# Kernel optimization log

Measured on AMD Instinct MI355X. Metric: run time of the kernel, lower is better.

## Reference

```python
import jax, jax.numpy as jnp
import numpy as np

N_NODES = 50000
D_IN = 128
HIDDEN = 128
UNITS_DENSE = 256
N_EDGES = 600000
N_PRED = 200000
N_SEL = 300000


def setup_inputs() -> dict:
    key = jax.random.key(0)
    ks = jax.random.split(key, 12)
    node_state = jax.random.normal(ks[0], (N_NODES, D_IN), jnp.float32)
    edge_index = jax.random.randint(ks[1], (2, N_EDGES), 0, N_NODES, jnp.int32)
    out_edges = jax.random.randint(ks[2], (2, N_PRED), 0, N_NODES, jnp.int32)
    set_idx = jnp.sort(jax.random.randint(ks[3], (N_SEL,), 0, 2 * N_PRED, jnp.int32))
    # Glorot-ish scaled weights
    W1 = jax.random.normal(ks[4], (D_IN, HIDDEN), jnp.float32) / np.float32(np.sqrt(D_IN))
    b1 = jnp.zeros((HIDDEN,), jnp.float32)
    W2 = jax.random.normal(ks[5], (HIDDEN, HIDDEN), jnp.float32) / np.float32(np.sqrt(HIDDEN))
    b2 = jnp.zeros((HIDDEN,), jnp.float32)
    dense_W = jax.random.normal(ks[6], (2 * 0 + HIDDEN, UNITS_DENSE), jnp.float32) / np.float32(np.sqrt(HIDDEN))
    dense_b = jnp.zeros((UNITS_DENSE,), jnp.float32)
    out_W = jax.random.normal(ks[7], (UNITS_DENSE, 2), jnp.float32) / np.float32(np.sqrt(UNITS_DENSE))
    out_b = jnp.zeros((2,), jnp.float32)
    return {
        "node_state": node_state, "edge_index": edge_index, "out_edges": out_edges,
        "set_idx": set_idx, "W1": W1, "b1": b1, "W2": W2, "b2": b2,
        "dense_W": dense_W, "dense_b": dense_b, "out_W": out_W, "out_b": out_b,
    }


def _graph_conv(h, src, dst, W, b):
    """DGL GraphConv, norm='both', no activation: D_in^{-1/2} A D_out^{-1/2} H W + b."""
    n = h.shape[0]
    ones = jnp.ones(src.shape[0], h.dtype)
    deg_out = jnp.clip(jax.ops.segment_sum(ones, src, num_segments=n), 1.0)  # [N]
    deg_in = jnp.clip(jax.ops.segment_sum(ones, dst, num_segments=n), 1.0)   # [N]
    h = (h * jax.lax.rsqrt(deg_out)[:, None]) @ W                            # [N, H]
    agg = jax.ops.segment_sum(h[src], dst, num_segments=n)                   # [N, H]
    return agg * jax.lax.rsqrt(deg_in)[:, None] + b


def reference(node_state, edge_index, out_edges, set_idx,
              W1, b1, W2, b2, dense_W, dense_b, out_W, out_b):
    src, dst = edge_index[0], edge_index[1]
    h = _graph_conv(node_state, src, dst, W1, b1)
    h = _graph_conv(h, src, dst, W2, b2)
    # concat along axis=0 as in the original: [2*E_pred, H]
    edge_state = jnp.concatenate([h[out_edges[0]], h[out_edges[1]]], axis=0)
    # boolean_mask replaced by equivalent gather of selected (True) rows
    edge_state_set = edge_state[set_idx]                                      # [N_SEL, H]
    hidden = jax.nn.relu(edge_state_set @ dense_W + dense_b)
    return jax.nn.softmax(hidden @ out_W + out_b, axis=-1)
```

## Files before the change

### kernel.cpp

```cpp
#include <hip/hip_runtime.h>

#define NN 50000
#define DD 128
#define NE 600000
#define NP 200000
#define NS 300000
#define NU 256
#define NBH 128
#define EPB 4688
#define NW 12500

typedef __attribute__((ext_vector_type(8))) short short8;
typedef __attribute__((ext_vector_type(4))) float floatx4;

__device__ inline float bf2f(unsigned int u16) {
    unsigned int x = u16 << 16;
    float f; __builtin_memcpy(&f, &x, 4); return f;
}
__device__ inline unsigned short f2bf(float f) {
    unsigned int x; __builtin_memcpy(&x, &f, 4);
    unsigned int lsb = (x >> 16) & 1u;
    x += 0x7fffu + lsb;
    return (unsigned short)(x >> 16);
}

__global__ __launch_bounds__(256) void k_hist(const int* __restrict__ ei,
                                              unsigned int* __restrict__ P) {
    __shared__ unsigned int hw[NW];
    int b = blockIdx.x, half = blockIdx.y, tid = threadIdx.x;
    for (int w = tid; w < NW; w += 256) hw[w] = 0;
    __syncthreads();
    const int* src = ei + (size_t)half * NE;
    int e0 = b * EPB, e1 = min(e0 + EPB, NE);
    for (int e = e0 + tid; e < e1; e += 256) {
        int s = src[e];
        atomicAdd(&hw[s >> 2], 1u << ((s & 3) * 8));
    }
    __syncthreads();
    unsigned int* Pb = P + ((size_t)half * NBH + b) * NW;
    for (int w = tid; w < NW; w += 256) Pb[w] = hw[w];
}

__global__ void k_reduce(const unsigned int* __restrict__ P, int* __restrict__ deg_in,
                         float* __restrict__ r) {
    int w = blockIdx.x * 256 + threadIdx.x;
    if (w >= 2 * NW) return;
    int half = (w >= NW);
    int wl = w - half * NW;
    const unsigned int* Ph = P + (size_t)half * NBH * NW + wl;
    int c0 = 0, c1 = 0, c2 = 0, c3 = 0;
    for (int b = 0; b < NBH; ++b) {
        unsigned int v = Ph[(size_t)b * NW];
        c0 += v & 0xff; c1 += (v >> 8) & 0xff; c2 += (v >> 16) & 0xff; c3 += v >> 24;
    }
    int nb = wl * 4;
    if (half) {
        int4 d = {c0, c1, c2, c3};
        *(int4*)(deg_in + nb) = d;
    }
    float4 rr = {rsqrtf((float)max(c0, 1)), rsqrtf((float)max(c1, 1)),
                 rsqrtf((float)max(c2, 1)), rsqrtf((float)max(c3, 1))};
    *(float4*)(r + (size_t)half * NN + nb) = rr;
}

__global__ __launch_bounds__(1024) void k_scan(const int* __restrict__ deg_in,
                                               int* __restrict__ row_ptr) {
    __shared__ int wsum[16];
    __shared__ int woff[16];
    __shared__ int carry_s;
    __shared__ int total_s;
    int tid = threadIdx.x, lane = tid & 63, w = tid >> 6;
    if (tid == 0) carry_s = 0;
    __syncthreads();
    for (int wb = 0; wb < NW; wb += 1024) {
        int i4 = wb + tid;
        int4 v = {0, 0, 0, 0};
        if (i4 < NW) v = *(const int4*)(deg_in + i4 * 4);
        int t0 = v.x, t1 = t0 + v.y, t2 = t1 + v.z, tot = t2 + v.w;
        int x = tot;
#pragma unroll
        for (int off = 1; off < 64; off <<= 1) {
            int y = __shfl_up(x, off);
            if (lane >= off) x += y;
        }
        if (lane == 63) wsum[w] = x;
        __syncthreads();
        if (w == 0 && lane < 16) {
            int s = wsum[lane];
            int xs = s;
#pragma unroll
            for (int off = 1; off < 16; off <<= 1) {
                int y = __shfl_up(xs, off);
                if (lane >= off) xs += y;
            }
            woff[lane] = xs - s;
            if (lane == 15) total_s = xs;
        }
        __syncthreads();
        if (i4 < NW) {
            int base = carry_s + woff[w] + x - tot;
            int4 o = {base, base + t0, base + t1, base + t2};
            *(int4*)(row_ptr + i4 * 4) = o;
        }
        __syncthreads();
        if (tid == 0) carry_s += total_s;
        __syncthreads();
    }
    if (tid == 0) row_ptr[NN] = carry_s;
}

__global__ void k_colscan(const unsigned int* __restrict__ Pin, const int* __restrict__ row_ptr,
                          int* __restrict__ basetab) {
    int n = blockIdx.x * 256 + threadIdx.x;
    if (n >= NN) return;
    int wl = n >> 2, sh = (n & 3) * 8;
    int run = row_ptr[n];
    for (int b = 0; b < NBH; ++b) {
        basetab[(size_t)b * NN + n] = run;
        run += (Pin[(size_t)b * NW + wl] >> sh) & 0xff;
    }
}

__global__ __launch_bounds__(256) void k_bucket2(const int* __restrict__ ei,
                                                 const int* __restrict__ basetab,
                                                 int* __restrict__ col) {
    __shared__ unsigned int cw[NW];
    int b = blockIdx.x, tid = threadIdx.x;
    for (int w = tid; w < NW; w += 256) cw[w] = 0;
    __syncthreads();
    const int* bt = basetab + (size_t)b * NN;
    int e0 = b * EPB, e1 = min(e0 + EPB, NE);
    for (int e = e0 + tid; e < e1; e += 256) {
        int s = ei[e], d = ei[NE + e];
        int sh = (d & 3) * 8;
        unsigned int old = atomicAdd(&cw[d >> 2], 1u << sh);
        int local = (old >> sh) & 0xff;
        col[bt[d] + local] = s;
    }
}

__global__ void k_castT(const float* __restrict__ src, unsigned short* __restrict__ dst,
                        int R, int C) {
    int t = blockIdx.x * 256 + threadIdx.x;
    if (t < R * C) {
        int r = t / C, c = t - r * C;
        dst[c * R + r] = f2bf(src[t]);
    }
}

template <bool ABF>
__global__ __launch_bounds__(256) void k_gemm_bf(const void* __restrict__ Ap,
                                                 const float* __restrict__ rs,
                                                 const unsigned short* __restrict__ BT,
                                                 unsigned short* __restrict__ Cm) {
    __shared__ unsigned short As[64][136];
    __shared__ unsigned short Bs[128][136];
    int tid = threadIdx.x, lane = tid & 63, wave = tid >> 6;
    int quad = lane >> 4, l16 = lane & 15;
    int row0 = blockIdx.x * 64;

    if (ABF) {
        const unsigned short* A = (const unsigned short*)Ap;
#pragma unroll
        for (int p = 0; p < 4; ++p) {
            int fid = tid + p * 256;
            int r = fid >> 4, c = fid & 15;
            int gr = row0 + r; if (gr > NN - 1) gr = NN - 1;
            *(uint4*)&As[r][c * 8] = *(const uint4*)(A + (size_t)gr * DD + c * 8);
        }
    } else {
        const float* A = (const float*)Ap;
#pragma unroll
        for (int p = 0; p < 8; ++p) {
            int fid = tid + p * 256;
            int r = fid >> 5, c = fid & 31;
            int gr = row0 + r; if (gr > NN - 1) gr = NN - 1;
            float4 v = *(const float4*)(A + (size_t)gr * DD + c * 4);
            ushort4 u;
            u.x = f2bf(v.x); u.y = f2bf(v.y); u.z = f2bf(v.z); u.w = f2bf(v.w);
            *(ushort4*)&As[r][c * 4] = u;
        }
    }
#pragma unroll
    for (int p = 0; p < 8; ++p) {
        int fid = tid + p * 256;
        int r = fid >> 4, c = fid & 15;
        *(uint4*)&Bs[r][c * 8] = *(const uint4*)(BT + (size_t)r * DD + c * 8);
    }
    __syncthreads();

    short8 af[4];
#pragma unroll
    for (int ks = 0; ks < 4; ++ks)
        af[ks] = *(const short8*)&As[wave * 16 + l16][ks * 32 + quad * 8];
    floatx4 acc[8];
#pragma unroll
    for (int nt = 0; nt < 8; ++nt) acc[nt] = (floatx4){0.f, 0.f, 0.f, 0.f};
#pragma unroll
    for (int ks = 0; ks < 4; ++ks) {
#pragma unroll
        for (int nt = 0; nt < 8; ++nt) {
            short8 bf = *(const short8*)&Bs[nt * 16 + l16][ks * 32 + quad * 8];
            acc[nt] = __builtin_amdgcn_mfma_f32_16x16x32_bf16(af[ks], bf, acc[nt], 0, 0, 0);
        }
    }
    int rbase = row0 + wave * 16 + quad * 4;
#pragma unroll
    for (int r = 0; r < 4; ++r) {
        int gr = rbase + r;
        if (gr < NN) {
            float s = rs[gr];
#pragma unroll
            for (int nt = 0; nt < 8; ++nt)
                Cm[(size_t)gr * DD + nt * 16 + l16] = f2bf(acc[nt][r] * s);
        }
    }
}

__global__ __launch_bounds__(256) void k_aggregate(const unsigned short* __restrict__ T,
                                                   const int* __restrict__ row_ptr,
                                                   const int* __restrict__ col,
                                                   const float* __restrict__ r_in,
                                                   const float* __restrict__ b,
                                                   unsigned short* __restrict__ H) {
    int node = blockIdx.x * 4 + (threadIdx.x >> 6);
    if (node >= NN) return;
    int lane = threadIdx.x & 63;
    int beg = row_ptr[node], end = row_ptr[node + 1];
    float a0 = 0.f, a1 = 0.f;
    for (int base = beg; base < end; base += 64) {
        int m = end - base; if (m > 64) m = 64;
        int myidx = (lane < m) ? col[base + lane] : 0;
        int j = 0;
        for (; j + 4 <= m; j += 4) {
            int s0 = __shfl(myidx, j), s1 = __shfl(myidx, j + 1);
            int s2 = __shfl(myidx, j + 2), s3 = __shfl(myidx, j + 3);
            unsigned int v0 = *(const unsigned int*)(T + (size_t)s0 * DD + lane * 2);
            unsigned int v1 = *(const unsigned int*)(T + (size_t)s1 * DD + lane * 2);
            unsigned int v2 = *(const unsigned int*)(T + (size_t)s2 * DD + lane * 2);
            unsigned int v3 = *(const unsigned int*)(T + (size_t)s3 * DD + lane * 2);
            a0 += bf2f(v0 & 0xffff) + bf2f(v1 & 0xffff) + bf2f(v2 & 0xffff) + bf2f(v3 & 0xffff);
            a1 += bf2f(v0 >> 16) + bf2f(v1 >> 16) + bf2f(v2 >> 16) + bf2f(v3 >> 16);
        }
        for (; j < m; ++j) {
            int s = __shfl(myidx, j);
            unsigned int v = *(const unsigned int*)(T + (size_t)s * DD + lane * 2);
            a0 += bf2f(v & 0xffff);
            a1 += bf2f(v >> 16);
        }
    }
    float rv = r_in[node];
    float o0 = a0 * rv + b[lane * 2];
    float o1 = a1 * rv + b[lane * 2 + 1];
    unsigned int packed = (unsigned int)f2bf(o0) | ((unsigned int)f2bf(o1) << 16);
    *(unsigned int*)(H + (size_t)node * DD + lane * 2) = packed;
}

__global__ __launch_bounds__(256) void k_mlp_mfma(const unsigned short* __restrict__ H2,
                                                  const unsigned short* __restrict__ BTd,
                                                  const float* __restrict__ db,
                                                  const float* __restrict__ oW,
                                                  const float* __restrict__ ob,
                                                  float* __restrict__ P) {
    __shared__ unsigned short As[64][136];
    __shared__ unsigned short Bs[128][136];
    int tid = threadIdx.x, lane = tid & 63, wave = tid >> 6;
    int quad = lane >> 4, l16 = lane & 15;
    int row0 = blockIdx.x * 64;
#pragma unroll
    for (int p = 0; p < 4; ++p) {
        int fid = tid + p * 256;
        int r = fid >> 4, c = fid & 15;
        int gr = row0 + r; if (gr > NN - 1) gr = NN - 1;
        *(uint4*)&As[r][c * 8] = *(const uint4*)(H2 + (size_t)gr * DD + c * 8);
    }
    short8 af[4];
    floatx4 acc[16];
#pragma unroll
    for (int i = 0; i < 16; ++i) acc[i] = (floatx4){0.f, 0.f, 0.f, 0.f};

    for (int ch = 0; ch < 2; ++ch) {
        __syncthreads();
#pragma unroll
        for (int p = 0; p < 8; ++p) {
            int fid = tid + p * 256;
            int r = fid >> 4, c = fid & 15;
            *(uint4*)&Bs[r][c * 8] = *(const uint4*)(BTd + (size_t)(ch * 128 + r) * DD + c * 8);
        }
        __syncthreads();
        if (ch == 0) {
#pragma unroll
            for (int ks = 0; ks < 4; ++ks)
                af[ks] = *(const short8*)&As[wave * 16 + l16][ks * 32 + quad * 8];
        }
#pragma unroll
        for (int ks = 0; ks < 4; ++ks) {
#pragma unroll
            for (int nt = 0; nt < 8; ++nt) {
                short8 bf = *(const short8*)&Bs[nt * 16 + l16][ks * 32 + quad * 8];
                acc[ch * 8 + nt] =
                    __builtin_amdgcn_mfma_f32_16x16x32_bf16(af[ks], bf, acc[ch * 8 + nt], 0, 0, 0);
            }
        }
    }
    int rbase = row0 + wave * 16 + quad * 4;
#pragma unroll
    for (int r = 0; r < 4; ++r) {
        float p0 = 0.f, p1 = 0.f;
#pragma unroll
        for (int ch = 0; ch < 2; ++ch) {
#pragma unroll
            for (int nt = 0; nt < 8; ++nt) {
                int colc = ch * 128 + nt * 16 + l16;
                float h = acc[ch * 8 + nt][r] + db[colc];
                h = fmaxf(h, 0.f);
                p0 += h * oW[2 * colc];
                p1 += h * oW[2 * colc + 1];
            }
        }
#pragma unroll
        for (int m = 8; m >= 1; m >>= 1) {
            p0 += __shfl_xor(p0, m, 16);
            p1 += __shfl_xor(p1, m, 16);
        }
        if (l16 == 0) {
            int gr = rbase + r;
            if (gr < NN) {
                float l0 = p0 + ob[0], l1 = p1 + ob[1];
                float mx = fmaxf(l0, l1);
                float e0 = __expf(l0 - mx), e1 = __expf(l1 - mx);
                float inv = 1.f / (e0 + e1);
                float2 pr = {e0 * inv, e1 * inv};
                *(float2*)(P + 2 * gr) = pr;
            }
        }
    }
}

__global__ void k_gather(const int* __restrict__ sidx, const int* __restrict__ oe,
                         const float* __restrict__ P, float* __restrict__ out) {
    int i = blockIdx.x * 256 + threadIdx.x;
    if (i >= NS) return;
    int node = oe[sidx[i]];
    float2 v = *(const float2*)(P + 2 * node);
    *(float2*)(out + 2 * i) = v;
}

extern "C" void kernel_launch(void* const* d_in, const int* in_sizes, int n_in,
                              void* d_out, int out_size, void* d_ws, size_t ws_size,
                              hipStream_t stream) {
    const float* node_state = (const float*)d_in[0];
    const int* ei   = (const int*)d_in[1];
    const int* oe   = (const int*)d_in[2];
    const int* sidx = (const int*)d_in[3];
    const float* W1 = (const float*)d_in[4];
    const float* b1 = (const float*)d_in[5];
    const float* W2 = (const float*)d_in[6];
    const float* b2 = (const float*)d_in[7];
    const float* dW = (const float*)d_in[8];
    const float* db = (const float*)d_in[9];
    const float* oW = (const float*)d_in[10];
    const float* ob = (const float*)d_in[11];
    float* out = (float*)d_out;

    char* ws = (char*)d_ws;
    size_t off = 0;
    auto carve = [&](size_t bytes) -> char* {
        char* p = ws + off;
        off = (off + bytes + 255) & ~(size_t)255;
        return p;
    };
    int*   deg_in  = (int*)carve((size_t)NN * 4);
    float* r       = (float*)carve((size_t)2 * NN * 4);
    int*   row_ptr = (int*)carve((size_t)(NN + 1) * 4);
    int*   col     = (int*)carve((size_t)NE * 4);
    unsigned int* P_hist = (unsigned int*)carve((size_t)2 * NBH * NW * 4);
    int*   basetab = (int*)carve((size_t)NBH * NN * 4);
    unsigned short* t   = (unsigned short*)carve((size_t)NN * DD * 2);
    unsigned short* h   = (unsigned short*)carve((size_t)NN * DD * 2);
    unsigned short* BT1 = (unsigned short*)carve((size_t)DD * DD * 2);
    unsigned short* BT2 = (unsigned short*)carve((size_t)DD * DD * 2);
    unsigned short* BTd = (unsigned short*)carve((size_t)DD * NU * 2);
    float* P = (float*)t;

    float* r_out = r;
    float* r_in  = r + NN;

    k_hist<<<dim3(NBH, 2), 256, 0, stream>>>(ei, P_hist);
    k_reduce<<<(2 * NW + 255) / 256, 256, 0, stream>>>(P_hist, deg_in, r);
    k_scan<<<1, 1024, 0, stream>>>(deg_in, row_ptr);
    k_colscan<<<(NN + 255) / 256, 256, 0, stream>>>(P_hist + (size_t)NBH * NW, row_ptr, basetab);
    k_bucket2<<<NBH, 256, 0, stream>>>(ei, basetab, col);

    k_castT<<<(DD * DD + 255) / 256, 256, 0, stream>>>(W1, BT1, DD, DD);
    k_castT<<<(DD * DD + 255) / 256, 256, 0, stream>>>(W2, BT2, DD, DD);
    k_castT<<<(DD * NU + 255) / 256, 256, 0, stream>>>(dW, BTd, DD, NU);

    k_gemm_bf<false><<<(NN + 63) / 64, 256, 0, stream>>>(node_state, r_out, BT1, t);
    k_aggregate<<<(NN + 3) / 4, 256, 0, stream>>>(t, row_ptr, col, r_in, b1, h);

    k_gemm_bf<true><<<(NN + 63) / 64, 256, 0, stream>>>(h, r_out, BT2, t);
    k_aggregate<<<(NN + 3) / 4, 256, 0, stream>>>(t, row_ptr, col, r_in, b2, h);

    k_mlp_mfma<<<(NN + 63) / 64, 256, 0, stream>>>(h, BTd, db, oW, ob, P);
    k_gather<<<(NS + 255) / 256, 256, 0, stream>>>(sidx, oe, P, out);
}
```

Measured before the change: 270.8 us.

## Fuse neighbor aggregation into following GEMM and MLP kernels; merge weight casts

The standalone aggregate kernels are removed. Each 64-row GEMM block now gathers and sums its own rows' neighbor features straight into shared memory, then runs the MFMA GEMM (layer-2 transform) or the dense MLP on them. This avoids writing the intermediate h to global memory and reading it back, and cuts the launch count; the three weight-cast kernels are also merged into one. The catch is fewer parallel waves during aggregation: 782 blocks of 4 waves, each wave handling 16 nodes serially, versus one wave per node before. That can lower the memory-level parallelism available for the latency-bound gather.

```diff
diff --git a/kernel.cpp b/kernel.cpp
--- a/kernel.cpp
+++ b/kernel.cpp
@@ -9,6 +9,7 @@
 #define NBH 128
 #define EPB 4688
 #define NW 12500
+#define NB64 782
 
 typedef __attribute__((ext_vector_type(8))) short short8;
 typedef __attribute__((ext_vector_type(4))) float floatx4;
@@ -139,47 +140,43 @@
     }
 }
 
-__global__ void k_castT(const float* __restrict__ src, unsigned short* __restrict__ dst,
-                        int R, int C) {
+__global__ void k_castW(const float* __restrict__ W1, const float* __restrict__ W2,
+                        const float* __restrict__ dW, unsigned short* __restrict__ BT1,
+                        unsigned short* __restrict__ BT2, unsigned short* __restrict__ BTd) {
     int t = blockIdx.x * 256 + threadIdx.x;
-    if (t < R * C) {
-        int r = t / C, c = t - r * C;
-        dst[c * R + r] = f2bf(src[t]);
-    }
-}
-
-template <bool ABF>
-__global__ __launch_bounds__(256) void k_gemm_bf(const void* __restrict__ Ap,
-                                                 const float* __restrict__ rs,
-                                                 const unsigned short* __restrict__ BT,
-                                                 unsigned short* __restrict__ Cm) {
+    if (t < 16384) {
+        int r = t >> 7, c = t & 127;
+        BT1[c * 128 + r] = f2bf(W1[t]);
+    } else if (t < 32768) {
+        int t2 = t - 16384;
+        int r = t2 >> 7, c = t2 & 127;
+        BT2[c * 128 + r] = f2bf(W2[t2]);
+    } else if (t < 65536) {
+        int t2 = t - 32768;
+        int r = t2 >> 8, c = t2 & 255;
+        BTd[c * 128 + r] = f2bf(dW[t2]);
+    }
+}
+
+__global__ __launch_bounds__(256) void k_gemm1(const float* __restrict__ A,
+                                               const float* __restrict__ rs,
+                                               const unsigned short* __restrict__ BT,
+                                               unsigned short* __restrict__ Cm) {
     __shared__ unsigned short As[64][136];
     __shared__ unsigned short Bs[128][136];
     int tid = threadIdx.x, lane = tid & 63, wave = tid >> 6;
     int quad = lane >> 4, l16 = lane & 15;
     int row0 = blockIdx.x * 64;
 
-    if (ABF) {
-        const unsigned short* A = (const unsigned short*)Ap;
-#pragma unroll
-        for (int p = 0; p < 4; ++p) {
-            int fid = tid + p * 256;
-            int r = fid >> 4, c = fid & 15;
-            int gr = row0 + r; if (gr > NN - 1) gr = NN - 1;
-            *(uint4*)&As[r][c * 8] = *(const uint4*)(A + (size_t)gr * DD + c * 8);
-        }
-    } else {
-        const float* A = (const float*)Ap;
-#pragma unroll
-        for (int p = 0; p < 8; ++p) {
-            int fid = tid + p * 256;
-            int r = fid >> 5, c = fid & 31;
-            int gr = row0 + r; if (gr > NN - 1) gr = NN - 1;
-            float4 v = *(const float4*)(A + (size_t)gr * DD + c * 4);
-            ushort4 u;
-            u.x = f2bf(v.x); u.y = f2bf(v.y); u.z = f2bf(v.z); u.w = f2bf(v.w);
-            *(ushort4*)&As[r][c * 4] = u;
-        }
+#pragma unroll
+    for (int p = 0; p < 8; ++p) {
+        int fid = tid + p * 256;
+        int r = fid >> 5, c = fid & 31;
+        int gr = row0 + r; if (gr > NN - 1) gr = NN - 1;
+        float4 v = *(const float4*)(A + (size_t)gr * DD + c * 4);
+        ushort4 u;
+        u.x = f2bf(v.x); u.y = f2bf(v.y); u.z = f2bf(v.z); u.w = f2bf(v.w);
+        *(ushort4*)&As[r][c * 4] = u;
     }
 #pragma unroll
     for (int p = 0; p < 8; ++p) {
@@ -217,90 +214,171 @@
     }
 }
 
-__global__ __launch_bounds__(256) void k_aggregate(const unsigned short* __restrict__ T,
-                                                   const int* __restrict__ row_ptr,
-                                                   const int* __restrict__ col,
-                                                   const float* __restrict__ r_in,
-                                                   const float* __restrict__ b,
-                                                   unsigned short* __restrict__ H) {
-    int node = blockIdx.x * 4 + (threadIdx.x >> 6);
-    if (node >= NN) return;
-    int lane = threadIdx.x & 63;
-    int beg = row_ptr[node], end = row_ptr[node + 1];
-    float a0 = 0.f, a1 = 0.f;
-    for (int base = beg; base < end; base += 64) {
-        int m = end - base; if (m > 64) m = 64;
-        int myidx = (lane < m) ? col[base + lane] : 0;
-        int j = 0;
-        for (; j + 4 <= m; j += 4) {
-            int s0 = __shfl(myidx, j), s1 = __shfl(myidx, j + 1);
-            int s2 = __shfl(myidx, j + 2), s3 = __shfl(myidx, j + 3);
-            unsigned int v0 = *(const unsigned int*)(T + (size_t)s0 * DD + lane * 2);
-            unsigned int v1 = *(const unsigned int*)(T + (size_t)s1 * DD + lane * 2);
-            unsigned int v2 = *(const unsigned int*)(T + (size_t)s2 * DD + lane * 2);
-            unsigned int v3 = *(const unsigned int*)(T + (size_t)s3 * DD + lane * 2);
-            a0 += bf2f(v0 & 0xffff) + bf2f(v1 & 0xffff) + bf2f(v2 & 0xffff) + bf2f(v3 & 0xffff);
-            a1 += bf2f(v0 >> 16) + bf2f(v1 >> 16) + bf2f(v2 >> 16) + bf2f(v3 >> 16);
-        }
-        for (; j < m; ++j) {
-            int s = __shfl(myidx, j);
-            unsigned int v = *(const unsigned int*)(T + (size_t)s * DD + lane * 2);
-            a0 += bf2f(v & 0xffff);
-            a1 += bf2f(v >> 16);
-        }
-    }
-    float rv = r_in[node];
-    float o0 = a0 * rv + b[lane * 2];
-    float o1 = a1 * rv + b[lane * 2 + 1];
-    unsigned int packed = (unsigned int)f2bf(o0) | ((unsigned int)f2bf(o1) << 16);
-    *(unsigned int*)(H + (size_t)node * DD + lane * 2) = packed;
-}
-
-__global__ __launch_bounds__(256) void k_mlp_mfma(const unsigned short* __restrict__ H2,
-                                                  const unsigned short* __restrict__ BTd,
-                                                  const float* __restrict__ db,
-                                                  const float* __restrict__ oW,
-                                                  const float* __restrict__ ob,
-                                                  float* __restrict__ P) {
+__device__ inline void agg_into_As(const unsigned short* __restrict__ T,
+                                   const int* __restrict__ row_ptr,
+                                   const int* __restrict__ col,
+                                   const float* __restrict__ r_in,
+                                   const float* __restrict__ bias,
+                                   unsigned short (*As)[136],
+                                   int row0, int lane, int wave) {
+    float2 breg = *(const float2*)(bias + lane * 2);
+#pragma unroll 1
+    for (int i = 0; i < 16; ++i) {
+        int node = row0 + wave * 16 + i;
+        int cn = min(node, NN - 1);
+        int beg = row_ptr[cn], end = row_ptr[cn + 1];
+        float a0 = 0.f, a1 = 0.f;
+        for (int base = beg; base < end; base += 64) {
+            int m = end - base; if (m > 64) m = 64;
+            int myidx = (lane < m) ? col[base + lane] : 0;
+            int j = 0;
+            for (; j + 4 <= m; j += 4) {
+                int s0 = __shfl(myidx, j), s1 = __shfl(myidx, j + 1);
+                int s2 = __shfl(myidx, j + 2), s3 = __shfl(myidx, j + 3);
+                unsigned int v0 = *(const unsigned int*)(T + (size_t)s0 * DD + lane * 2);
+                unsigned int v1 = *(const unsigned int*)(T + (size_t)s1 * DD + lane * 2);
+                unsigned int v2 = *(const unsigned int*)(T + (size_t)s2 * DD + lane * 2);
+                unsigned int v3 = *(const unsigned int*)(T + (size_t)s3 * DD + lane * 2);
+                a0 += bf2f(v0 & 0xffff) + bf2f(v1 & 0xffff) + bf2f(v2 & 0xffff) + bf2f(v3 & 0xffff);
+                a1 += bf2f(v0 >> 16) + bf2f(v1 >> 16) + bf2f(v2 >> 16) + bf2f(v3 >> 16);
+            }
+            for (; j < m; ++j) {
+                int s = __shfl(myidx, j);
+                unsigned int v = *(const unsigned int*)(T + (size_t)s * DD + lane * 2);
+                a0 += bf2f(v & 0xffff);
+                a1 += bf2f(v >> 16);
+            }
+        }
+        float rv = r_in[cn];
+        unsigned int packed = (unsigned int)f2bf(a0 * rv + breg.x) |
+                              ((unsigned int)f2bf(a1 * rv + breg.y) << 16);
+        *(unsigned int*)&As[wave * 16 + i][lane * 2] = packed;
+    }
+}
+
+__global__ __launch_bounds__(256) void k_agg_gemm(const unsigned short* __restrict__ T,
+                                                  const int* __restrict__ row_ptr,
+                                                  const int* __restrict__ col,
+                                                  const float* __restrict__ r_in,
+                                                  const float* __restrict__ bias,
+                                                  const float* __restrict__ rs,
+                                                  const unsigned short* __restrict__ BT,
+                                                  unsigned short* __restrict__ Cm) {
     __shared__ unsigned short As[64][136];
     __shared__ unsigned short Bs[128][136];
     int tid = threadIdx.x, lane = tid & 63, wave = tid >> 6;
     int quad = lane >> 4, l16 = lane & 15;
     int row0 = blockIdx.x * 64;
-#pragma unroll
-    for (int p = 0; p < 4; ++p) {
-        int fid = tid + p * 256;
-        int r = fid >> 4, c = fid & 15;
-        int gr = row0 + r; if (gr > NN - 1) gr = NN - 1;
-        *(uint4*)&As[r][c * 8] = *(const uint4*)(H2 + (size_t)gr * DD + c * 8);
-    }
+
+    uint4 breg[8];
+#pragma unroll
+    for (int p = 0; p < 8; ++p) {
+        int fid = tid + p * 256;
+        int r = fid >> 4, c = fid & 15;
+        breg[p] = *(const uint4*)(BT + (size_t)r * DD + c * 8);
+    }
+
+    agg_into_As(T, row_ptr, col, r_in, bias, As, row0, lane, wave);
+
+#pragma unroll
+    for (int p = 0; p < 8; ++p) {
+        int fid = tid + p * 256;
+        int r = fid >> 4, c = fid & 15;
+        *(uint4*)&Bs[r][c * 8] = breg[p];
+    }
+    __syncthreads();
+
     short8 af[4];
+#pragma unroll
+    for (int ks = 0; ks < 4; ++ks)
+        af[ks] = *(const short8*)&As[wave * 16 + l16][ks * 32 + quad * 8];
+    floatx4 acc[8];
+#pragma unroll
+    for (int nt = 0; nt < 8; ++nt) acc[nt] = (floatx4){0.f, 0.f, 0.f, 0.f};
+#pragma unroll
+    for (int ks = 0; ks < 4; ++ks) {
+#pragma unroll
+        for (int nt = 0; nt < 8; ++nt) {
+            short8 bf = *(const short8*)&Bs[nt * 16 + l16][ks * 32 + quad * 8];
+            acc[nt] = __builtin_amdgcn_mfma_f32_16x16x32_bf16(af[ks], bf, acc[nt], 0, 0, 0);
+        }
+    }
+    int rbase = row0 + wave * 16 + quad * 4;
+#pragma unroll
+    for (int r = 0; r < 4; ++r) {
+        int gr = rbase + r;
+        if (gr < NN) {
+            float s = rs[gr];
+#pragma unroll
+            for (int nt = 0; nt < 8; ++nt)
+                Cm[(size_t)gr * DD + nt * 16 + l16] = f2bf(acc[nt][r] * s);
+        }
+    }
+}
+
+__global__ __launch_bounds__(256) void k_agg_mlp(const unsigned short* __restrict__ T,
+                                                 const int* __restrict__ row_ptr,
+                                                 const int* __restrict__ col,
+                                                 const float* __restrict__ r_in,
+                                                 const float* __restrict__ bias,
+                                                 const unsigned short* __restrict__ BTd,
+                                                 const float* __restrict__ db,
+                                                 const float* __restrict__ oW,
+                                                 const float* __restrict__ ob,
+                                                 float* __restrict__ P) {
+    __shared__ unsigned short As[64][136];
+    __shared__ unsigned short Bs[128][136];
+    int tid = threadIdx.x, lane = tid & 63, wave = tid >> 6;
+    int quad = lane >> 4, l16 = lane & 15;
+    int row0 = blockIdx.x * 64;
+
+    uint4 breg[8];
+#pragma unroll
+    for (int p = 0; p < 8; ++p) {
+        int fid = tid + p * 256;
+        int r = fid >> 4, c = fid & 15;
+        breg[p] = *(const uint4*)(BTd + (size_t)r * DD + c * 8);
+    }
+
+    agg_into_As(T, row_ptr, col, r_in, bias, As, row0, lane, wave);
+
+#pragma unroll
+    for (int p = 0; p < 8; ++p) {
+        int fid = tid + p * 256;
+        int r = fid >> 4, c = fid & 15;
+        *(uint4*)&Bs[r][c * 8] = breg[p];
+    }
+    __syncthreads();
+
+    short8 af[4];
+#pragma unroll
+    for (int ks = 0; ks < 4; ++ks)
+        af[ks] = *(const short8*)&As[wave * 16 + l16][ks * 32 + quad * 8];
     floatx4 acc[16];
 #pragma unroll
     for (int i = 0; i < 16; ++i) acc[i] = (floatx4){0.f, 0.f, 0.f, 0.f};
-
-    for (int ch = 0; ch < 2; ++ch) {
-        __syncthreads();
-#pragma unroll
-        for (int p = 0; p < 8; ++p) {
-            int fid = tid + p * 256;
-            int r = fid >> 4, c = fid & 15;
-            *(uint4*)&Bs[r][c * 8] = *(const uint4*)(BTd + (size_t)(ch * 128 + r) * DD + c * 8);
-        }
-        __syncthreads();
-        if (ch == 0) {
-#pragma unroll
-            for (int ks = 0; ks < 4; ++ks)
-                af[ks] = *(const short8*)&As[wave * 16 + l16][ks * 32 + quad * 8];
-        }
-#pragma unroll
-        for (int ks = 0; ks < 4; ++ks) {
-#pragma unroll
-            for (int nt = 0; nt < 8; ++nt) {
-                short8 bf = *(const short8*)&Bs[nt * 16 + l16][ks * 32 + quad * 8];
-                acc[ch * 8 + nt] =
-                    __builtin_amdgcn_mfma_f32_16x16x32_bf16(af[ks], bf, acc[ch * 8 + nt], 0, 0, 0);
-            }
+#pragma unroll
+    for (int ks = 0; ks < 4; ++ks) {
+#pragma unroll
+        for (int nt = 0; nt < 8; ++nt) {
+            short8 bf = *(const short8*)&Bs[nt * 16 + l16][ks * 32 + quad * 8];
+            acc[nt] = __builtin_amdgcn_mfma_f32_16x16x32_bf16(af[ks], bf, acc[nt], 0, 0, 0);
+        }
+    }
+    __syncthreads();
+#pragma unroll
+    for (int p = 0; p < 8; ++p) {
+        int fid = tid + p * 256;
+        int r = fid >> 4, c = fid & 15;
+        *(uint4*)&Bs[r][c * 8] = *(const uint4*)(BTd + (size_t)(128 + r) * DD + c * 8);
+    }
+    __syncthreads();
+#pragma unroll
+    for (int ks = 0; ks < 4; ++ks) {
+#pragma unroll
+        for (int nt = 0; nt < 8; ++nt) {
+            short8 bf = *(const short8*)&Bs[nt * 16 + l16][ks * 32 + quad * 8];
+            acc[8 + nt] = __builtin_amdgcn_mfma_f32_16x16x32_bf16(af[ks], bf, acc[8 + nt], 0, 0, 0);
         }
     }
     int rbase = row0 + wave * 16 + quad * 4;
@@ -377,7 +455,7 @@
     unsigned int* P_hist = (unsigned int*)carve((size_t)2 * NBH * NW * 4);
     int*   basetab = (int*)carve((size_t)NBH * NN * 4);
     unsigned short* t   = (unsigned short*)carve((size_t)NN * DD * 2);
-    unsigned short* h   = (unsigned short*)carve((size_t)NN * DD * 2);
+    unsigned short* t2  = (unsigned short*)carve((size_t)NN * DD * 2);
     unsigned short* BT1 = (unsigned short*)carve((size_t)DD * DD * 2);
     unsigned short* BT2 = (unsigned short*)carve((size_t)DD * DD * 2);
     unsigned short* BTd = (unsigned short*)carve((size_t)DD * NU * 2);
@@ -392,16 +470,11 @@
     k_colscan<<<(NN + 255) / 256, 256, 0, stream>>>(P_hist + (size_t)NBH * NW, row_ptr, basetab);
     k_bucket2<<<NBH, 256, 0, stream>>>(ei, basetab, col);
 
-    k_castT<<<(DD * DD + 255) / 256, 256, 0, stream>>>(W1, BT1, DD, DD);
-    k_castT<<<(DD * DD + 255) / 256, 256, 0, stream>>>(W2, BT2, DD, DD);
-    k_castT<<<(DD * NU + 255) / 256, 256, 0, stream>>>(dW, BTd, DD, NU);
-
-    k_gemm_bf<false><<<(NN + 63) / 64, 256, 0, stream>>>(node_state, r_out, BT1, t);
-    k_aggregate<<<(NN + 3) / 4, 256, 0, stream>>>(t, row_ptr, col, r_in, b1, h);
-
-    k_gemm_bf<true><<<(NN + 63) / 64, 256, 0, stream>>>(h, r_out, BT2, t);
-    k_aggregate<<<(NN + 3) / 4, 256, 0, stream>>>(t, row_ptr, col, r_in, b2, h);
-
-    k_mlp_mfma<<<(NN + 63) / 64, 256, 0, stream>>>(h, BTd, db, oW, ob, P);
+    k_castW<<<256, 256, 0, stream>>>(W1, W2, dW, BT1, BT2, BTd);
+
+    k_gemm1<<<NB64, 256, 0, stream>>>(node_state, r_out, BT1, t);
+    k_agg_gemm<<<NB64, 256, 0, stream>>>(t, row_ptr, col, r_in, b1, r_out, BT2, t2);
+    k_agg_mlp<<<NB64, 256, 0, stream>>>(t2, row_ptr, col, r_in, b2, BTd, db, oW, ob, P);
+
     k_gather<<<(NS + 255) / 256, 256, 0, stream>>>(sidx, oe, P, out);
 }
```

New measurement: 352.1 us. 30.0% more time.
